# Kernel optimization log

Measured on AMD Instinct MI355X. Metric: run time of the kernel, lower is better.

Reference implementation:

```python
import jax, jax.numpy as jnp
import numpy as np

B, T, D, H, W = 2, 8192, 512, 8, 256
d = D // H  # 64
NC = T // W  # number of chunks (T divisible by W)


def setup_inputs() -> dict:
    key = jax.random.key(0)
    ks = jax.random.split(key, 9)
    s = 1.0 / np.sqrt(D).astype(np.float32)
    x = jax.random.normal(ks[0], (B, T, D), jnp.float32)
    Wq = jax.random.normal(ks[1], (D, D), jnp.float32) * s
    Wk = jax.random.normal(ks[2], (D, D), jnp.float32) * s
    Wv = jax.random.normal(ks[3], (D, D), jnp.float32) * s
    Wo = jax.random.normal(ks[4], (D, D), jnp.float32) * s
    bq = jax.random.normal(ks[5], (D,), jnp.float32) * 0.01
    bk = jax.random.normal(ks[6], (D,), jnp.float32) * 0.01
    bv = jax.random.normal(ks[7], (D,), jnp.float32) * 0.01
    bo = jax.random.normal(ks[8], (D,), jnp.float32) * 0.01
    return {"x": x, "Wq": Wq, "bq": bq, "Wk": Wk, "bk": bk,
            "Wv": Wv, "bv": bv, "Wo": Wo, "bo": bo}


def _local_attention(q, k, v):
    # q, k, v: [B, H, T, d]. Each W-sized query chunk attends to keys in
    # [chunk_start - W, chunk_end + W) -> a 3W window, masked at boundaries.
    qc = q.reshape(B, H, NC, W, d)
    pad = ((0, 0), (0, 0), (W, W), (0, 0))
    kp = jnp.pad(k, pad)
    vp = jnp.pad(v, pad)
    # window gather indices into padded sequence: [NC, 3W]
    pos = jnp.arange(NC)[:, None] * W + jnp.arange(3 * W)[None, :]
    kw = kp[:, :, pos, :]  # [B, H, NC, 3W, d]
    vw = vp[:, :, pos, :]  # [B, H, NC, 3W, d]
    valid = (pos >= W) & (pos < T + W)  # [NC, 3W] true for real (unpadded) keys
    scores = jnp.einsum('bhcqd,bhckd->bhcqk', qc, kw) * (d ** -0.5)
    scores = jnp.where(valid[None, None, :, None, :], scores, -jnp.inf)
    attn = jax.nn.softmax(scores, axis=-1)
    out = jnp.einsum('bhcqk,bhckd->bhcqd', attn, vw)
    return out.reshape(B, H, T, d)


def reference(x, Wq, bq, Wk, bk, Wv, bv, Wo, bo):
    # Linear = x @ W.T + b (torch nn.Linear convention)
    q = (x @ Wq.T + bq).reshape(B, T, H, d).transpose(0, 2, 1, 3)
    # k_proj / v_proj run under torch.no_grad() in the original
    k = jax.lax.stop_gradient(x @ Wk.T + bk).reshape(B, T, H, d).transpose(0, 2, 1, 3)
    v = jax.lax.stop_gradient(x @ Wv.T + bv).reshape(B, T, H, d).transpose(0, 2, 1, 3)
    out = _local_attention(q, k, v)           # [B, H, T, d]
    out = out.transpose(0, 2, 1, 3).reshape(B, T, D)
    return out @ Wo.T + bo
```

## Files before the change

kernel.cpp:

```cpp
#include <hip/hip_runtime.h>
#include <hip/hip_bf16.h>

typedef unsigned short u16;
typedef unsigned int   u32;
typedef __bf16 bf16x8 __attribute__((ext_vector_type(8)));
typedef float  f32x4  __attribute__((ext_vector_type(4)));

#define BB 2
#define TT 8192
#define DD 512
#define HH 8
#define WW 256
#define DH 64
#define NX 8388608
#define NW 262144

__device__ __forceinline__ float b2f(u16 u) {
    unsigned int x = ((unsigned int)u) << 16;
    return __builtin_bit_cast(float, x);
}
__device__ __forceinline__ u16 f2b(float f) {
    __bf16 h = (__bf16)f;
    return __builtin_bit_cast(u16, h);
}
__device__ __forceinline__ bf16x8 ldsfrag(const u16* p) {
    return *(const bf16x8*)p;
}
__device__ __forceinline__ f32x4 mfma16(bf16x8 a, bf16x8 b, f32x4 c) {
    return __builtin_amdgcn_mfma_f32_16x16x32_bf16(a, b, c, 0, 0, 0);
}

typedef __attribute__((address_space(1))) u32 gu32;
typedef __attribute__((address_space(3))) u32 lu32;
__device__ __forceinline__ void gl_lds(const u16* g, u16* l) {
    __builtin_amdgcn_global_load_lds((gu32*)g, (lu32*)l, 16, 0, 0);
}

__device__ __forceinline__ void cvt8(const void* s, u16* d, long i, int f) {
    if (f) {
        const u32* sp = (const u32*)s + i;
        uint4 a = *(const uint4*)(sp);
        uint4 b = *(const uint4*)(sp + 4);
        u16 o[8];
        o[0] = f2b(__builtin_bit_cast(float, a.x));
        o[1] = f2b(__builtin_bit_cast(float, a.y));
        o[2] = f2b(__builtin_bit_cast(float, a.z));
        o[3] = f2b(__builtin_bit_cast(float, a.w));
        o[4] = f2b(__builtin_bit_cast(float, b.x));
        o[5] = f2b(__builtin_bit_cast(float, b.y));
        o[6] = f2b(__builtin_bit_cast(float, b.z));
        o[7] = f2b(__builtin_bit_cast(float, b.w));
        *(uint4*)(d + i) = *(const uint4*)o;
    } else {
        *(uint4*)(d + i) = *(const uint4*)((const u16*)s + i);
    }
}

__global__ void convert_all(const void* x, const void* Wq, const void* bq,
                            const void* Wk, const void* bk, const void* Wv,
                            const void* bv, const void* Wo, const void* bo,
                            u16* __restrict__ xb, u16* __restrict__ Wcat,
                            u16* __restrict__ Wob, u16* __restrict__ bcat,
                            u16* __restrict__ bob, int* __restrict__ flagw)
{
    __shared__ int sflag;
    const int tid = threadIdx.x;
    if (tid == 0) sflag = 0;
    __syncthreads();
    int mybad = 0;
    for (int i = tid; i < 2048; i += 256) {
        float v = b2f(((const u16*)x)[i]);
        if (!(fabsf(v) < 100.f)) mybad = 1;
    }
    if (mybad) atomicOr(&sflag, 1);
    __syncthreads();
    const int f = sflag ? 1 : 0;
    if (blockIdx.x == 0 && tid == 0) *flagw = f;

    long i = ((long)blockIdx.x * 256 + tid) * 8;
    if (i < NX)            { cvt8(x,  xb,           i, f); return; }
    i -= NX;
    if (i < NW)            { cvt8(Wq, Wcat,         i, f); return; }
    i -= NW;
    if (i < NW)            { cvt8(Wk, Wcat + NW,    i, f); return; }
    i -= NW;
    if (i < NW)            { cvt8(Wv, Wcat + 2*NW,  i, f); return; }
    i -= NW;
    if (i < NW)            { cvt8(Wo, Wob,          i, f); return; }
    i -= NW;
    if (i < 512)           { cvt8(bq, bcat,         i, f); return; }
    i -= 512;
    if (i < 512)           { cvt8(bk, bcat + 512,   i, f); return; }
    i -= 512;
    if (i < 512)           { cvt8(bv, bcat + 1024,  i, f); return; }
    i -= 512;
    if (i < 512)           { cvt8(bo, bob,          i, f); }
}

__global__ __launch_bounds__(512, 2)
void gemm256(const u16* __restrict__ A, const u16* __restrict__ Bw,
             const u16* __restrict__ bias, void* __restrict__ out0,
             u16* __restrict__ out1, u16* __restrict__ out2,
             int mode, const int* __restrict__ flagp)
{
    __shared__ __align__(16) u16 AsF[3][256 * 64];
    __shared__ __align__(16) u16 BsF[3][128 * 64];

    const int tid  = threadIdx.x;
    const int lane = tid & 63;
    const int wv   = tid >> 6;
    const int col  = lane & 15;
    const int quad = lane >> 4;
    const int wm   = (wv >> 1) * 64;
    const int wn   = (wv & 1) * 64;
    const int m0   = blockIdx.x * 256;
    const int n0   = blockIdx.y * 128;

    f32x4 acc[4][4] = {};

    const int lr  = lane >> 3;
    const int lc  = lane & 7;
    const int cbs = lc ^ lr;

    auto STG = [&](int buf, int k0, int half) {
        #pragma unroll
        for (int i = 0; i < 2; i++) {
            const int g = wv * 4 + half * 2 + i;
            gl_lds(A + (size_t)(m0 + g * 8 + lr) * 512 + k0 + cbs * 8,
                   &AsF[buf][g * 512]);
        }
        const int g2 = wv * 2 + half;
        gl_lds(Bw + (size_t)(n0 + g2 * 8 + lr) * 512 + k0 + cbs * 8,
               &BsF[buf][g2 * 512]);
    };

    STG(0, 0, 0);  STG(0, 0, 1);
    STG(1, 64, 0); STG(1, 64, 1);
    asm volatile("s_waitcnt vmcnt(6)" ::: "memory");
    __builtin_amdgcn_s_barrier();
    __builtin_amdgcn_sched_barrier(0);

    #pragma unroll
    for (int t = 0; t < 8; t++) {
        const int p  = t % 3;
        const int q  = (t + 2) % 3;
        const int k2 = (t + 2) * 64;
        bf16x8 fa[2][4], fb[2][4];
        #pragma unroll
        for (int mi = 0; mi < 4; mi++)
            fa[0][mi] = ldsfrag(&AsF[p][(wm + mi * 16 + col) * 64 + ((0 + quad) ^ (col & 7)) * 8]);
        #pragma unroll
        for (int ni = 0; ni < 4; ni++)
            fb[0][ni] = ldsfrag(&BsF[p][(wn + ni * 16 + col) * 64 + ((0 + quad) ^ (col & 7)) * 8]);
        if (t < 6) STG(q, k2, 0);
        #pragma unroll
        for (int mi = 0; mi < 4; mi++)
            fa[1][mi] = ldsfrag(&AsF[p][(wm + mi * 16 + col) * 64 + ((4 + quad) ^ (col & 7)) * 8]);
        #pragma unroll
        for (int ni = 0; ni < 4; ni++)
            fb[1][ni] = ldsfrag(&BsF[p][(wn + ni * 16 + col) * 64 + ((4 + quad) ^ (col & 7)) * 8]);
        if (t < 6) STG(q, k2, 1);
        asm volatile("s_waitcnt lgkmcnt(0)" ::: "memory");
        __builtin_amdgcn_sched_barrier(0);
        __builtin_amdgcn_s_setprio(1);
        #pragma unroll
        for (int kk = 0; kk < 2; kk++)
            #pragma unroll
            for (int mi = 0; mi < 4; mi++)
                #pragma unroll
                for (int ni = 0; ni < 4; ni++)
                    acc[mi][ni] = mfma16(fa[kk][mi], fb[kk][ni], acc[mi][ni]);
        __builtin_amdgcn_s_setprio(0);
        if (t < 6)      asm volatile("s_waitcnt vmcnt(6)" ::: "memory");
        else if (t == 6) asm volatile("s_waitcnt vmcnt(0)" ::: "memory");
        if (t < 7) {
            __builtin_amdgcn_s_barrier();
            __builtin_amdgcn_sched_barrier(0);
        }
    }

    if (mode == 0) {
        #pragma unroll
        for (int ni = 0; ni < 4; ni++) {
            const int gn = n0 + wn + ni * 16 + col;
            const float bv = b2f(bias[gn]);
            const int seg = gn >> 9;
            #pragma unroll
            for (int mi = 0; mi < 4; mi++) {
                const int gmb = m0 + wm + mi * 16 + quad * 4;
                if (seg < 2) {
                    u16* dst = (seg == 0) ? (u16*)out0 : out1;
                    #pragma unroll
                    for (int r = 0; r < 4; r++)
                        dst[(size_t)(gmb + r) * 512 + (gn & 511)] = f2b(acc[mi][ni][r] + bv);
                } else {
                    const int d = gn & 63, hh = (gn >> 6) & 7;
                    const int bb = gmb >> 13, t = gmb & 8191;
                    u16 pb[4];
                    #pragma unroll
                    for (int r = 0; r < 4; r++) pb[r] = f2b(acc[mi][ni][r] + bv);
                    uint2 pk;
                    pk.x = pb[0] | ((u32)pb[1] << 16);
                    pk.y = pb[2] | ((u32)pb[3] << 16);
                    *(uint2*)&out2[((size_t)(bb * 8 + hh) * 64 + d) * 8192 + t] = pk;
                }
            }
        }
    } else {
        const int outf32 = *flagp;
        #pragma unroll
        for (int ni = 0; ni < 4; ni++) {
            const int gn = n0 + wn + ni * 16 + col;
            const float bv = b2f(bias[gn]);
            #pragma unroll
            for (int mi = 0; mi < 4; mi++) {
                #pragma unroll
                for (int r = 0; r < 4; r++) {
                    const int gm = m0 + wm + mi * 16 + quad * 4 + r;
                    const float v = acc[mi][ni][r] + bv;
                    if (outf32) ((float*)out0)[(size_t)gm * 512 + gn] = v;
                    else        ((u16*)out0)[(size_t)gm * 512 + gn]  = f2b(v);
                }
            }
        }
    }
}

#define PSW 72
__global__ __launch_bounds__(512, 4)
void attn_local(const u16* __restrict__ Qg, const u16* __restrict__ Kg,
                const u16* __restrict__ VTg, u16* __restrict__ Og)
{
    __shared__ __align__(16) u16 Ks[2][64 * 64];
    __shared__ __align__(16) u16 VTs[2][64 * 64];
    __shared__ __align__(16) u16 Ps[8][32 * PSW];

    const int tid  = threadIdx.x;
    const int lane = tid & 63;
    const int wv   = tid >> 6;
    const int col  = lane & 15;
    const int quad = lane >> 4;

    const int idx = blockIdx.x;
    const int c = idx & 31;
    const int h = (idx >> 5) & 7;
    const int b = idx >> 8;

    const int t0 = c * WW;
    const int wq = wv * 32;

    const int sc_lo = (c == 0) ? 4 : 0;
    const int nsc   = (c == 0 || c == 31) ? 8 : 12;

    const int ldr = lane >> 3;
    const int ldc = lane & 7;

    bf16x8 qf[2][2];
    {
        const size_t qbase = ((size_t)(b * TT + t0 + wq + col)) * DD + h * DH + quad * 8;
        #pragma unroll
        for (int qi = 0; qi < 2; qi++)
            #pragma unroll
            for (int kk = 0; kk < 2; kk++)
                qf[qi][kk] = *(const bf16x8*)(Qg + qbase + (size_t)qi * 16 * DD + kk * 32);
    }

    f32x4 o[4][2] = {};
    float lsum[2] = {0.f, 0.f};

    u16* psb = &Ps[wv][0];

    {
        const int kstart = t0 - WW + sc_lo * 64;
        const int rr = wv * 8 + ldr;
        const int cb = ldc ^ (rr & 7);
        gl_lds(Kg  + ((size_t)(b * TT + kstart + rr)) * DD + h * DH + cb * 8,
               &Ks[0][wv * 512]);
        gl_lds(VTg + ((size_t)((b * HH + h) * DH + rr)) * TT + kstart + cb * 8,
               &VTs[0][wv * 512]);
    }

    for (int it = 0; it < nsc; it++) {
        __syncthreads();
        if (it + 1 < nsc) {
            const int kstart = t0 - WW + (sc_lo + it + 1) * 64;
            const int buf = (it + 1) & 1;
            const int rr = wv * 8 + ldr;
            const int cb = ldc ^ (rr & 7);
            gl_lds(Kg  + ((size_t)(b * TT + kstart + rr)) * DD + h * DH + cb * 8,
                   &Ks[buf][wv * 512]);
            gl_lds(VTg + ((size_t)((b * HH + h) * DH + rr)) * TT + kstart + cb * 8,
                   &VTs[buf][wv * 512]);
        }
        const u16* ks = &Ks[it & 1][0];
        const u16* vs = &VTs[it & 1][0];

        f32x4 s[4][2];
        #pragma unroll
        for (int ns = 0; ns < 4; ns++)
            #pragma unroll
            for (int qi = 0; qi < 2; qi++)
                s[ns][qi] = (f32x4){0.f, 0.f, 0.f, 0.f};
        #pragma unroll
        for (int ns = 0; ns < 4; ns++) {
            const int row = ns * 16 + col;
            bf16x8 ka0 = ldsfrag(&ks[row * 64 + ((0 + quad) ^ (col & 7)) * 8]);
            bf16x8 ka1 = ldsfrag(&ks[row * 64 + ((4 + quad) ^ (col & 7)) * 8]);
            #pragma unroll
            for (int qi = 0; qi < 2; qi++) {
                s[ns][qi] = mfma16(ka0, qf[qi][0], s[ns][qi]);
                s[ns][qi] = mfma16(ka1, qf[qi][1], s[ns][qi]);
            }
        }

        #pragma unroll
        for (int ns = 0; ns < 4; ns++) {
            #pragma unroll
            for (int qi = 0; qi < 2; qi++) {
                u16 pb[4];
                #pragma unroll
                for (int r = 0; r < 4; r++) {
                    const float p = __expf(s[ns][qi][r] * 0.125f);
                    pb[r] = f2b(p);
                    lsum[qi] += p;
                }
                uint2 pk;
                pk.x = pb[0] | ((u32)pb[1] << 16);
                pk.y = pb[2] | ((u32)pb[3] << 16);
                *(uint2*)&psb[(qi * 16 + col) * PSW + ns * 16 + quad * 4] = pk;
            }
        }
        asm volatile("" ::: "memory");

        #pragma unroll
        for (int kt = 0; kt < 2; kt++) {
            bf16x8 pf[2];
            #pragma unroll
            for (int qi = 0; qi < 2; qi++)
                pf[qi] = ldsfrag(&psb[(qi * 16 + col) * PSW + kt * 32 + quad * 8]);
            #pragma unroll
            for (int di = 0; di < 4; di++) {
                bf16x8 va = ldsfrag(&vs[(di * 16 + col) * 64 + ((kt * 4 + quad) ^ (col & 7)) * 8]);
                #pragma unroll
                for (int qi = 0; qi < 2; qi++)
                    o[di][qi] = mfma16(va, pf[qi], o[di][qi]);
            }
        }
    }

    #pragma unroll
    for (int qi = 0; qi < 2; qi++) {
        float l = lsum[qi];
        l += __shfl_xor(l, 16);
        l += __shfl_xor(l, 32);
        lsum[qi] = 1.0f / l;
    }

    #pragma unroll
    for (int qi = 0; qi < 2; qi++) {
        const size_t ob = ((size_t)(b * TT + t0 + wq + qi * 16 + col)) * DD + h * DH + quad * 4;
        #pragma unroll
        for (int di = 0; di < 4; di++) {
            u16 pb[4];
            #pragma unroll
            for (int r = 0; r < 4; r++) pb[r] = f2b(o[di][qi][r] * lsum[qi]);
            uint2 pk;
            pk.x = pb[0] | ((u32)pb[1] << 16);
            pk.y = pb[2] | ((u32)pb[3] << 16);
            *(uint2*)&Og[ob + di * 16] = pk;
        }
    }
}

extern "C" void kernel_launch(void* const* d_in, const int* in_sizes, int n_in,
                              void* d_out, int out_size, void* d_ws, size_t ws_size,
                              hipStream_t stream)
{
    u16* ws   = (u16*)d_ws;
    u16* xb   = ws;
    u16* Wcat = xb + NX;
    u16* Wob  = Wcat + 3 * NW;
    u16* bcat = Wob + NW;
    u16* bob  = bcat + 1536;
    u16* qws  = bob + 512;
    u16* kws  = qws + NX;
    u16* vtws = kws + NX;
    u16* aws  = vtws + NX;
    int* flag = (int*)(aws + NX);

    convert_all<<<4609, 256, 0, stream>>>(
        d_in[0], d_in[1], d_in[2], d_in[3], d_in[4], d_in[5], d_in[6], d_in[7], d_in[8],
        xb, Wcat, Wob, bcat, bob, flag);

    gemm256<<<dim3(64, 12), 512, 0, stream>>>(xb, Wcat, bcat, qws, kws, vtws, 0, flag);
    attn_local<<<dim3(BB * HH * 32), 512, 0, stream>>>(qws, kws, vtws, aws);
    gemm256<<<dim3(64, 4), 512, 0, stream>>>(aws, Wob, bob, d_out, nullptr, nullptr, 1, flag);
}
```

Measured before the change: 195.3 us.

## Keep softmax probabilities in registers instead of staging through LDS

Removes the per-wave LDS buffer for P. The probability fragments from the QK^T MFMA output are packed directly into the B-operand layout of the PV MFMA. This works by permuting the key dimension: the V^T fragment is now gathered from two 8-byte LDS reads whose key ordering matches the register layout of P. It also interleaves the score and PV computation in two halves. The aim is to drop LDS write/read traffic and the LDS footprint, at the cost of narrower 8-byte V reads, which may add bank conflicts or instructions.

```diff
diff --git a/kernel.cpp b/kernel.cpp
--- a/kernel.cpp
+++ b/kernel.cpp
@@ -226,14 +226,12 @@
     }
 }
 
-#define PSW 72
 __global__ __launch_bounds__(512, 4)
 void attn_local(const u16* __restrict__ Qg, const u16* __restrict__ Kg,
                 const u16* __restrict__ VTg, u16* __restrict__ Og)
 {
     __shared__ __align__(16) u16 Ks[2][64 * 64];
     __shared__ __align__(16) u16 VTs[2][64 * 64];
-    __shared__ __align__(16) u16 Ps[8][32 * PSW];
 
     const int tid  = threadIdx.x;
     const int lane = tid & 63;
@@ -267,8 +265,6 @@
 
     f32x4 o[4][2] = {};
     float lsum[2] = {0.f, 0.f};
-
-    u16* psb = &Ps[wv][0];
 
     {
         const int kstart = t0 - WW + sc_lo * 64;
@@ -295,52 +291,50 @@
         const u16* ks = &Ks[it & 1][0];
         const u16* vs = &VTs[it & 1][0];
 
-        f32x4 s[4][2];
-        #pragma unroll
-        for (int ns = 0; ns < 4; ns++)
-            #pragma unroll
-            for (int qi = 0; qi < 2; qi++)
-                s[ns][qi] = (f32x4){0.f, 0.f, 0.f, 0.f};
-        #pragma unroll
-        for (int ns = 0; ns < 4; ns++) {
-            const int row = ns * 16 + col;
-            bf16x8 ka0 = ldsfrag(&ks[row * 64 + ((0 + quad) ^ (col & 7)) * 8]);
-            bf16x8 ka1 = ldsfrag(&ks[row * 64 + ((4 + quad) ^ (col & 7)) * 8]);
+        #pragma unroll
+        for (int half = 0; half < 2; half++) {
+            uint2 p2[2][2];
+            #pragma unroll
+            for (int nsl = 0; nsl < 2; nsl++) {
+                const int ns = half * 2 + nsl;
+                const int row = ns * 16 + col;
+                bf16x8 ka0 = ldsfrag(&ks[row * 64 + ((0 + quad) ^ (col & 7)) * 8]);
+                bf16x8 ka1 = ldsfrag(&ks[row * 64 + ((4 + quad) ^ (col & 7)) * 8]);
+                #pragma unroll
+                for (int qi = 0; qi < 2; qi++) {
+                    f32x4 sv = (f32x4){0.f, 0.f, 0.f, 0.f};
+                    sv = mfma16(ka0, qf[qi][0], sv);
+                    sv = mfma16(ka1, qf[qi][1], sv);
+                    u16 pb[4];
+                    #pragma unroll
+                    for (int r = 0; r < 4; r++) {
+                        const float p = __expf(sv[r] * 0.125f);
+                        pb[r] = f2b(p);
+                        lsum[qi] += p;
+                    }
+                    p2[nsl][qi].x = pb[0] | ((u32)pb[1] << 16);
+                    p2[nsl][qi].y = pb[2] | ((u32)pb[3] << 16);
+                }
+            }
+            bf16x8 pf[2];
             #pragma unroll
             for (int qi = 0; qi < 2; qi++) {
-                s[ns][qi] = mfma16(ka0, qf[qi][0], s[ns][qi]);
-                s[ns][qi] = mfma16(ka1, qf[qi][1], s[ns][qi]);
-            }
-        }
-
-        #pragma unroll
-        for (int ns = 0; ns < 4; ns++) {
-            #pragma unroll
-            for (int qi = 0; qi < 2; qi++) {
-                u16 pb[4];
-                #pragma unroll
-                for (int r = 0; r < 4; r++) {
-                    const float p = __expf(s[ns][qi][r] * 0.125f);
-                    pb[r] = f2b(p);
-                    lsum[qi] += p;
-                }
-                uint2 pk;
-                pk.x = pb[0] | ((u32)pb[1] << 16);
-                pk.y = pb[2] | ((u32)pb[3] << 16);
-                *(uint2*)&psb[(qi * 16 + col) * PSW + ns * 16 + quad * 4] = pk;
-            }
-        }
-        asm volatile("" ::: "memory");
-
-        #pragma unroll
-        for (int kt = 0; kt < 2; kt++) {
-            bf16x8 pf[2];
-            #pragma unroll
-            for (int qi = 0; qi < 2; qi++)
-                pf[qi] = ldsfrag(&psb[(qi * 16 + col) * PSW + kt * 32 + quad * 8]);
+                uint4 w;
+                w.x = p2[0][qi].x; w.y = p2[0][qi].y;
+                w.z = p2[1][qi].x; w.w = p2[1][qi].y;
+                pf[qi] = __builtin_bit_cast(bf16x8, w);
+            }
+            const int glo = (half * 4 +     (quad >> 1)) ^ (col & 7);
+            const int ghi = (half * 4 + 2 + (quad >> 1)) ^ (col & 7);
+            const int hb  = (quad & 1) * 8;
             #pragma unroll
             for (int di = 0; di < 4; di++) {
-                bf16x8 va = ldsfrag(&vs[(di * 16 + col) * 64 + ((kt * 4 + quad) ^ (col & 7)) * 8]);
+                const char* rowp = (const char*)&vs[(di * 16 + col) * 64];
+                uint2 lo = *(const uint2*)(rowp + glo * 16 + hb);
+                uint2 hi = *(const uint2*)(rowp + ghi * 16 + hb);
+                uint4 w4;
+                w4.x = lo.x; w4.y = lo.y; w4.z = hi.x; w4.w = hi.y;
+                bf16x8 va = __builtin_bit_cast(bf16x8, w4);
                 #pragma unroll
                 for (int qi = 0; qi < 2; qi++)
                     o[di][qi] = mfma16(va, pf[qi], o[di][qi]);
```

After: 192.9 us, median of 3. About the same (-1.2%).
